# Optimization experiments

Measured on AMD Instinct MI355X. Metric: run time of the kernel, lower is better.

The kernel has to match this reference:

```python
import jax, jax.numpy as jnp
import numpy as np

EPS = 1e-3  # keras LayerNormalization default epsilon


def layer_norm(x, g, b):
    mu = jnp.mean(x, axis=-1, keepdims=True)
    var = jnp.mean(jnp.square(x - mu), axis=-1, keepdims=True)
    return g * (x - mu) / jnp.sqrt(var + EPS) + b


def setup_inputs() -> dict:
    key = jax.random.key(0)
    ks = jax.random.split(key, 16)
    B, S, E, H, F = 2, 4096, 512, 8, 2048
    s_e = 1.0 / np.sqrt(E)
    s_f = 1.0 / np.sqrt(F)
    inp = {
        "x": jax.random.normal(ks[0], (B, S, E), dtype=jnp.float32),
        "WQ": jax.random.normal(ks[1], (E, E), dtype=jnp.float32) * s_e,
        "bQ": jnp.zeros((E,), jnp.float32),
        "WK": jax.random.normal(ks[2], (E, E), dtype=jnp.float32) * s_e,
        "bK": jnp.zeros((E,), jnp.float32),
        "WV": jax.random.normal(ks[3], (E, E), dtype=jnp.float32) * s_e,
        "bV": jnp.zeros((E,), jnp.float32),
        "WO": jax.random.normal(ks[4], (E, E), dtype=jnp.float32) * s_e,
        "bO": jnp.zeros((E,), jnp.float32),
        "W1": jax.random.normal(ks[5], (E, F), dtype=jnp.float32) * s_e,
        "b1": jnp.zeros((F,), jnp.float32),
        "W2": jax.random.normal(ks[6], (F, E), dtype=jnp.float32) * s_f,
        "b2": jnp.zeros((E,), jnp.float32),
        "g1": jnp.ones((E,), jnp.float32),
        "beta1": jnp.zeros((E,), jnp.float32),
        "g2": jnp.ones((E,), jnp.float32),
        "beta2": jnp.zeros((E,), jnp.float32),
        "num_head": 8,
    }
    return inp


def reference(x, WQ, bQ, WK, bK, WV, bV, WO, bO, W1, b1, W2, b2,
              g1, beta1, g2, beta2, num_head):
    B, S, E = x.shape
    H = num_head
    d = E // H
    scale = jnp.sqrt(jnp.asarray(d, jnp.float32))

    q = (x @ WQ + bQ).reshape(B, S, H, d).transpose(0, 2, 1, 3)  # [B,H,S,d]
    k = (x @ WK + bK).reshape(B, S, H, d).transpose(0, 2, 1, 3)
    v = (x @ WV + bV).reshape(B, S, H, d).transpose(0, 2, 1, 3)

    score = jnp.einsum('bhqd,bhkd->bhqk', q, k) / scale  # O(S^2) materialized, as in source
    attn = jax.nn.softmax(score, axis=-1)
    zs = jnp.einsum('bhqk,bhkd->bhqd', attn, v)  # [B,H,S,d]

    # Faithful to source bug: reshape [B,H,S,d] -> [B,S,E] WITHOUT transposing back
    zs = zs.reshape(B, S, E)
    zs = zs @ WO + bO

    z = layer_norm(zs + x, g1, beta1)
    r = jax.nn.relu(z @ W1 + b1) @ W2 + b2
    r = layer_norm(r + z, g2, beta2)
    return r
```

## Files before the change

### kernel.cpp

```cpp
#include <hip/hip_runtime.h>
#include <hip/hip_bf16.h>

typedef unsigned short u16;
typedef __attribute__((ext_vector_type(8))) short bf16x8;
typedef __attribute__((ext_vector_type(4))) float f32x4;
typedef __attribute__((ext_vector_type(16))) float f32x16;

static constexpr int BB = 2;
static constexpr int SS = 4096;
static constexpr int EE = 512;
static constexpr int HH = 8;
static constexpr int DD = 64;
static constexpr int FF = 2048;
static constexpr int NR = BB * SS;
static constexpr int QS = 3 * EE;

#define QSCALE 0.18033688011112042f

__device__ __forceinline__ u16 f2bf(float f) {
  union { float f; unsigned u; } v; v.f = f;
  unsigned r = v.u + 0x7FFFu + ((v.u >> 16) & 1u);
  return (u16)(r >> 16);
}
__device__ __forceinline__ unsigned pack2(float a, float b) {
  return (unsigned)f2bf(a) | ((unsigned)f2bf(b) << 16);
}
__device__ __forceinline__ float bf2f_lo(unsigned u) {
  union { unsigned u; float f; } v; v.u = u << 16; return v.f;
}
__device__ __forceinline__ float bf2f_hi(unsigned u) {
  union { unsigned u; float f; } v; v.u = u & 0xffff0000u; return v.f;
}
__device__ __forceinline__ unsigned cvtpk(float lo, float hi) {
  unsigned r;
  asm("v_cvt_pk_bf16_f32 %0, %1, %2" : "=v"(r) : "v"(lo), "v"(hi));
  return r;
}
__device__ __forceinline__ void perm32swap(unsigned& a, unsigned& b) {
  asm("v_permlane32_swap_b32 %0, %1" : "+v"(a), "+v"(b));
}
__device__ __forceinline__ void gload_lds16(const u16* g, u16* l) {
  __builtin_amdgcn_global_load_lds(
      (const __attribute__((address_space(1))) unsigned*)g,
      (__attribute__((address_space(3))) unsigned*)l, 16, 0, 0);
}

struct TrJob { const float* W; u16* Wt; int K, N, k0, n0; };

__device__ __forceinline__ void transp_tile(const float* W, u16* Wt, int K,
                                            int N, int k0, int n0, int t) {
  __shared__ float T[64][65];
  const int tn = t & 63, tk = t >> 6;
#pragma unroll
  for (int i = 0; i < 16; ++i) {
    int kk = tk * 16 + i;
    T[kk][tn] = W[(size_t)(k0 + kk) * N + n0 + tn];
  }
  __syncthreads();
#pragma unroll
  for (int i = 0; i < 16; ++i) {
    int nn = tk * 16 + i;
    Wt[(size_t)(n0 + nn) * K + k0 + tn] = f2bf(T[tn][nn]);
  }
}

__global__ __launch_bounds__(256) void prep_all(
    const float* __restrict__ x, u16* __restrict__ xb,
    const float* __restrict__ WQ, const float* __restrict__ WK,
    const float* __restrict__ WV, const float* __restrict__ WO,
    const float* __restrict__ W1, const float* __restrict__ W2,
    u16* __restrict__ Wqkv_t, u16* __restrict__ WO_t, u16* __restrict__ W1_t,
    u16* __restrict__ W2_t, const float* __restrict__ bQ,
    const float* __restrict__ bK, const float* __restrict__ bV,
    float* __restrict__ bqkv) {
  const int bx = blockIdx.x;
  const int t = threadIdx.x;
  if (bx < 2048) {
    int i = (bx * 256 + t) * 8;
    float4 a = *(const float4*)(x + i);
    float4 b = *(const float4*)(x + i + 4);
    uint4 u;
    u.x = pack2(a.x, a.y); u.y = pack2(a.z, a.w);
    u.z = pack2(b.x, b.y); u.w = pack2(b.z, b.w);
    *(uint4*)(xb + i) = u;
    return;
  }
  int idx = bx - 2048;
  if (idx < 768) {
    TrJob j;
    if (idx < 256) {
      const float* srcs[4] = {WQ, WK, WV, WO};
      u16* dsts[4] = {Wqkv_t, Wqkv_t + 512 * 512, Wqkv_t + 1024 * 512, WO_t};
      int w = idx >> 6, l = idx & 63;
      j = {srcs[w], dsts[w], 512, 512, (l & 7) * 64, (l >> 3) * 64};
    } else if (idx < 512) {
      int l = idx - 256;
      j = {W1, W1_t, 512, 2048, (l & 7) * 64, (l >> 3) * 64};
    } else {
      int l = idx - 512;
      j = {W2, W2_t, 2048, 512, (l & 31) * 64, (l >> 5) * 64};
    }
    transp_tile(j.W, j.Wt, j.K, j.N, j.k0, j.n0, t);
    return;
  }
  for (int i = t; i < QS; i += 256)
    bqkv[i] = i < 512 ? bQ[i] : (i < 1024 ? bK[i - 512] : bV[i - 1024]);
}

__global__ __launch_bounds__(256) void transp_v(const u16* __restrict__ qkvb,
                                                u16* __restrict__ vt) {
  __shared__ u16 T[64][72];
  const int s0 = blockIdx.x * 64, c0 = blockIdx.y * 64, b = blockIdx.z;
  const int t = threadIdx.x;
#pragma unroll
  for (int i = 0; i < 2; ++i) {
    int idx = t + i * 256;
    int row = idx >> 3, c8 = idx & 7;
    *(uint4*)(&T[row][c8 * 8]) = *(const uint4*)(
        &qkvb[((size_t)b * SS + s0 + row) * QS + 1024 + c0 + c8 * 8]);
  }
  __syncthreads();
#pragma unroll
  for (int i = 0; i < 2; ++i) {
    int idx = t + i * 256;
    int c = idx >> 3, s8 = idx & 7;
    u16 tmp[8];
#pragma unroll
    for (int j = 0; j < 8; ++j) tmp[j] = T[s8 * 8 + j][c];
    *(uint4*)(&vt[((size_t)b * EE + c0 + c) * SS + s0 + s8 * 8]) =
        *(uint4*)tmp;
  }
}

template <int RELU, int OUT_BF16, int SCALEQ = 0>
__global__ __launch_bounds__(256) void gemm64(
    const u16* __restrict__ A, const u16* __restrict__ Bt,
    const float* __restrict__ bias, void* __restrict__ Cout,
    int M, int N, int K) {
  __shared__ __align__(16) u16 As[2][64 * 64];
  __shared__ __align__(16) u16 Bs[2][64 * 64];
  const int t = threadIdx.x;
  const int lane = t & 63, wid = t >> 6;
  const int lm = lane & 15, lg = lane >> 4;
  const int bm = blockIdx.x * 64, bn = blockIdx.y * 64;
  const int wr = (wid >> 1) * 32, wc = (wid & 1) * 32;
  const int sr = lane >> 3;
  const int scb = (lane & 7) ^ sr;

  f32x4 acc[2][2];
#pragma unroll
  for (int i = 0; i < 2; ++i)
#pragma unroll
    for (int j = 0; j < 2; ++j) acc[i][j] = (f32x4){0.f, 0.f, 0.f, 0.f};

  auto stage = [&](int kb, int buf) {
#pragma unroll
    for (int i = 0; i < 2; ++i) {
      int r8 = wid * 16 + i * 8;
      gload_lds16(A + (size_t)(bm + r8 + sr) * K + kb + scb * 8,
                  &As[buf][r8 * 64]);
      gload_lds16(Bt + (size_t)(bn + r8 + sr) * K + kb + scb * 8,
                  &Bs[buf][r8 * 64]);
    }
  };

  stage(0, 0);
  const int nsteps = K >> 6;
  for (int s = 0; s < nsteps; ++s) {
    const int cur = s & 1;
    if (s + 1 < nsteps) {
      stage((s + 1) << 6, cur ^ 1);
      asm volatile("s_waitcnt vmcnt(4)" ::: "memory");
    } else {
      asm volatile("s_waitcnt vmcnt(0)" ::: "memory");
    }
    __builtin_amdgcn_sched_barrier(0);
    __builtin_amdgcn_s_barrier();

#pragma unroll
    for (int c = 0; c < 2; ++c) {
      bf16x8 af[2], bfr[2];
#pragma unroll
      for (int i = 0; i < 2; ++i) {
        int ar = wr + i * 16 + lm;
        af[i] = *(const bf16x8*)(
            &As[cur][ar * 64 + (((c * 4 + lg) ^ (ar & 7)) << 3)]);
        int br = wc + i * 16 + lm;
        bfr[i] = *(const bf16x8*)(
            &Bs[cur][br * 64 + (((c * 4 + lg) ^ (br & 7)) << 3)]);
      }
#pragma unroll
      for (int i = 0; i < 2; ++i)
#pragma unroll
        for (int j = 0; j < 2; ++j)
          acc[i][j] = __builtin_amdgcn_mfma_f32_16x16x32_bf16(
              af[i], bfr[j], acc[i][j], 0, 0, 0);
    }

    asm volatile("s_waitcnt lgkmcnt(0)" ::: "memory");
    __builtin_amdgcn_s_barrier();
  }

  float bi[2];
#pragma unroll
  for (int j = 0; j < 2; ++j) bi[j] = bias[bn + wc + j * 16 + lm];

#pragma unroll
  for (int i = 0; i < 2; ++i) {
#pragma unroll
    for (int j = 0; j < 2; ++j) {
      int col = bn + wc + j * 16 + lm;
#pragma unroll
      for (int r = 0; r < 4; ++r) {
        int row = bm + wr + i * 16 + lg * 4 + r;
        float vv = acc[i][j][r] + bi[j];
        if (RELU) vv = fmaxf(vv, 0.f);
        if (SCALEQ && col < 512) vv *= QSCALE;
        if (OUT_BF16)
          ((u16*)Cout)[(size_t)row * N + col] = f2bf(vv);
        else
          ((float*)Cout)[(size_t)row * N + col] = vv;
      }
    }
  }
}

__global__ __launch_bounds__(128, 4) void attn_split(
    const u16* __restrict__ qkv, const u16* __restrict__ vt,
    u16* __restrict__ po, float* __restrict__ pl) {
  __shared__ __align__(16) u16 K_lds[2][32 * 64];
  __shared__ __align__(16) u16 V_lds[2][64 * 32];

  const int bh = blockIdx.x;
  const int qblock = blockIdx.y;
  const int half = blockIdx.z;
  po += (size_t)half * (9u << 19);
  pl += (size_t)half * (1u << 18);
  const int b = bh >> 3, h = bh & 7;
  const int t = threadIdx.x;
  const int lane = t & 63, wid = t >> 6;
  const int q32 = lane & 31, hi = lane >> 5;
  const int qs7 = q32 & 7;
  const int vswz = (q32 & 3) ^ ((q32 >> 2) & 3);
  const size_t bS = (size_t)b * SS;
  const int koff0 = half * 2048;
  const u16* kp = qkv + 512;
  const u16* vrow = vt + ((size_t)b * EE + h * DD) * SS;
  const int qbase = qblock * 64 + wid * 32;

  bf16x8 qf[4];
  {
    const u16* qrow = qkv + (bS + qbase + q32) * QS + h * DD + hi * 8;
#pragma unroll
    for (int c = 0; c < 4; ++c) qf[c] = *(const bf16x8*)(qrow + c * 16);
  }

  const int sr = lane >> 3;
  const int scb = (lane & 7) ^ sr;
  const int vr = lane >> 2;
  const int vcb = (lane & 3) ^ (vr & 3) ^ ((vr >> 2) & 3);

  f32x16 o0, o1, z16;
#pragma unroll
  for (int i = 0; i < 16; ++i) { o0[i] = 0.f; o1[i] = 0.f; z16[i] = 0.f; }
  float lsum = 0.f;

  auto stage = [&](int kt, int bufi) {
#pragma unroll
    for (int i = 0; i < 2; ++i) {
      int rb = wid * 16 + i * 8;
      gload_lds16(
          kp + (bS + koff0 + kt * 32 + rb + sr) * QS + h * DD + scb * 8,
          &K_lds[bufi][rb * 64]);
    }
#pragma unroll
    for (int i = 0; i < 2; ++i) {
      int rb = wid * 32 + i * 16;
      gload_lds16(vrow + (size_t)(rb + vr) * SS + koff0 + kt * 32 + vcb * 8,
                  &V_lds[bufi][rb * 32]);
    }
  };

  stage(0, 0);

  constexpr int NT = 2048 / 32;
  for (int kt = 0; kt < NT; ++kt) {
    const int cur = kt & 1;
    if (kt + 1 < NT) {
      stage(kt + 1, cur ^ 1);
      asm volatile("s_waitcnt vmcnt(4)" ::: "memory");
    } else {
      asm volatile("s_waitcnt vmcnt(0)" ::: "memory");
    }
    __builtin_amdgcn_sched_barrier(0);
    __builtin_amdgcn_s_barrier();

    f32x16 s;
    __builtin_amdgcn_s_setprio(1);
    {
      bf16x8 kf = *(const bf16x8*)(
          &K_lds[cur][q32 * 64 + ((hi ^ qs7) << 3)]);
      s = __builtin_amdgcn_mfma_f32_32x32x16_bf16(kf, qf[0], z16, 0, 0, 0);
    }
#pragma unroll
    for (int c = 1; c < 4; ++c) {
      bf16x8 kf = *(const bf16x8*)(
          &K_lds[cur][q32 * 64 + (((2 * c + hi) ^ qs7) << 3)]);
      s = __builtin_amdgcn_mfma_f32_32x32x16_bf16(kf, qf[c], s, 0, 0, 0);
    }
    __builtin_amdgcn_s_setprio(0);
    float p[16];
#pragma unroll
    for (int r = 0; r < 16; ++r) {
      p[r] = __builtin_amdgcn_exp2f(s[r]);
      lsum += p[r];
    }

    __builtin_amdgcn_s_setprio(1);
#pragma unroll
    for (int kc = 0; kc < 2; ++kc) {
      const int rA = kc * 8, rB = rA + 4;
      unsigned wA0 = cvtpk(p[rA + 0], p[rA + 1]);
      unsigned wA1 = cvtpk(p[rA + 2], p[rA + 3]);
      unsigned wB0 = cvtpk(p[rB + 0], p[rB + 1]);
      unsigned wB1 = cvtpk(p[rB + 2], p[rB + 3]);
      perm32swap(wA0, wB0);
      perm32swap(wA1, wB1);
      union { unsigned u[4]; bf16x8 v; } pf;
      pf.u[0] = wA0; pf.u[1] = wA1; pf.u[2] = wB0; pf.u[3] = wB1;
      bf16x8 vf0 = *(const bf16x8*)(
          &V_lds[cur][q32 * 32 + (((2 * kc + hi) ^ vswz) << 3)]);
      bf16x8 vf1 = *(const bf16x8*)(
          &V_lds[cur][(32 + q32) * 32 + (((2 * kc + hi) ^ vswz) << 3)]);
      o0 = __builtin_amdgcn_mfma_f32_32x32x16_bf16(pf.v, vf0, o0, 0, 0, 0);
      o1 = __builtin_amdgcn_mfma_f32_32x32x16_bf16(pf.v, vf1, o1, 0, 0, 0);
    }
    __builtin_amdgcn_s_setprio(0);

    asm volatile("s_waitcnt lgkmcnt(0)" ::: "memory");
    __builtin_amdgcn_s_barrier();
  }

  float fl = lsum + __shfl_xor(lsum, 32);
  const size_t rowbase = (size_t)bh * 4096 + qbase;
  if (lane < 32) pl[rowbase + q32] = fl;
#pragma unroll
  for (int reg = 0; reg < 16; ++reg) {
    int q = (reg & 3) + 8 * (reg >> 2) + 4 * hi;
    u16* dst = po + (rowbase + q) * 64;
    dst[q32] = f2bf(o0[reg]);
    dst[32 + q32] = f2bf(o1[reg]);
  }
}

__global__ __launch_bounds__(256) void attn_combine(
    const u16* __restrict__ po0, const u16* __restrict__ po1,
    const float* __restrict__ pl0, const float* __restrict__ pl1,
    u16* __restrict__ zs) {
  const int row = blockIdx.x * 32 + (threadIdx.x >> 3);
  const int dblk = (threadIdx.x & 7) * 8;
  const int bh = row >> 12, s = row & 4095;
  const int b = bh >> 3, h = bh & 7;
  const float inv = 1.f / (pl0[row] + pl1[row]);
  uint4 a = *(const uint4*)(po0 + (size_t)row * 64 + dblk);
  uint4 c = *(const uint4*)(po1 + (size_t)row * 64 + dblk);
  uint4 r;
  r.x = pack2((bf2f_lo(a.x) + bf2f_lo(c.x)) * inv,
              (bf2f_hi(a.x) + bf2f_hi(c.x)) * inv);
  r.y = pack2((bf2f_lo(a.y) + bf2f_lo(c.y)) * inv,
              (bf2f_hi(a.y) + bf2f_hi(c.y)) * inv);
  r.z = pack2((bf2f_lo(a.z) + bf2f_lo(c.z)) * inv,
              (bf2f_hi(a.z) + bf2f_hi(c.z)) * inv);
  r.w = pack2((bf2f_lo(a.w) + bf2f_lo(c.w)) * inv,
              (bf2f_hi(a.w) + bf2f_hi(c.w)) * inv);
  u16* dst = zs + ((size_t)b * SS + h * 512 + (s >> 3)) * EE + (s & 7) * 64;
  *(uint4*)(dst + dblk) = r;
}

template <int WF32>
__global__ __launch_bounds__(128) void add_ln_b(
    const u16* __restrict__ a, const u16* __restrict__ xres,
    const float* __restrict__ g, const float* __restrict__ beta,
    u16* __restrict__ outb, float* __restrict__ outf) {
  const int row = blockIdx.x;
  const int tid = threadIdx.x;
  uint2 av = *(const uint2*)(a + (size_t)row * EE + tid * 4);
  uint2 xv = *(const uint2*)(xres + (size_t)row * EE + tid * 4);
  float vx = bf2f_lo(av.x) + bf2f_lo(xv.x);
  float vy = bf2f_hi(av.x) + bf2f_hi(xv.x);
  float vz = bf2f_lo(av.y) + bf2f_lo(xv.y);
  float vw = bf2f_hi(av.y) + bf2f_hi(xv.y);
  float sum = vx + vy + vz + vw;
  float sq = vx * vx + vy * vy + vz * vz + vw * vw;
#pragma unroll
  for (int off = 1; off < 64; off <<= 1) {
    sum += __shfl_xor(sum, off);
    sq += __shfl_xor(sq, off);
  }
  __shared__ float s0[2], s1[2];
  int w = tid >> 6;
  if ((tid & 63) == 0) { s0[w] = sum; s1[w] = sq; }
  __syncthreads();
  sum = s0[0] + s0[1];
  sq = s1[0] + s1[1];
  float mu = sum * (1.0f / EE);
  float var = sq * (1.0f / EE) - mu * mu;
  float r = rsqrtf(var + 1e-3f);
  int c = tid * 4;
  float4 gv = *(const float4*)(g + c);
  float4 bv = *(const float4*)(beta + c);
  float o0 = gv.x * (vx - mu) * r + bv.x;
  float o1 = gv.y * (vy - mu) * r + bv.y;
  float o2 = gv.z * (vz - mu) * r + bv.z;
  float o3 = gv.w * (vw - mu) * r + bv.w;
  if (WF32) {
    float4 ov = {o0, o1, o2, o3};
    *(float4*)(outf + (size_t)row * EE + c) = ov;
  } else {
    uint2 u;
    u.x = pack2(o0, o1);
    u.y = pack2(o2, o3);
    *(uint2*)(outb + (size_t)row * EE + c) = u;
  }
}

extern "C" void kernel_launch(void* const* d_in, const int* in_sizes, int n_in,
                              void* d_out, int out_size, void* d_ws,
                              size_t ws_size, hipStream_t stream) {
  const float* x = (const float*)d_in[0];
  const float* WQ = (const float*)d_in[1];
  const float* bQ = (const float*)d_in[2];
  const float* WK = (const float*)d_in[3];
  const float* bK = (const float*)d_in[4];
  const float* WV = (const float*)d_in[5];
  const float* bV = (const float*)d_in[6];
  const float* WO = (const float*)d_in[7];
  const float* bO = (const float*)d_in[8];
  const float* W1 = (const float*)d_in[9];
  const float* b1 = (const float*)d_in[10];
  const float* W2 = (const float*)d_in[11];
  const float* b2 = (const float*)d_in[12];
  const float* g1 = (const float*)d_in[13];
  const float* be1 = (const float*)d_in[14];
  const float* g2 = (const float*)d_in[15];
  const float* be2 = (const float*)d_in[16];
  float* out = (float*)d_out;

  const size_t MB = 1u << 20;
  char* w = (char*)d_ws;
  u16* Wqkv_t = (u16*)(w + 0);
  u16* WO_t   = (u16*)(w + 2 * MB);
  u16* W1_t   = (u16*)(w + 3 * MB);
  u16* W2_t   = (u16*)(w + 5 * MB);
  float* bqkv = (float*)(w + 7 * MB);
  u16* qkvb = (u16*)(w + 8 * MB);
  u16* zsb  = (u16*)(w + 32 * MB);
  u16* po0  = (u16*)(w + 40 * MB);
  u16* po1  = (u16*)(w + 49 * MB);
  float* pl0 = (float*)(w + 58 * MB);
  float* pl1 = (float*)(w + 59 * MB);
  u16* zs2b = (u16*)(w + 40 * MB);
  u16* f2b  = (u16*)(w + 49 * MB);
  u16* zb   = (u16*)(w + 72 * MB);
  u16* xb   = (u16*)(w + 80 * MB);
  u16* vtb  = (u16*)(w + 88 * MB);
  u16* f1   = (u16*)(w + 8 * MB);

  dim3 blk(256);

  prep_all<<<dim3(2817), blk, 0, stream>>>(x, xb, WQ, WK, WV, WO, W1, W2,
                                           Wqkv_t, WO_t, W1_t, W2_t, bQ, bK,
                                           bV, bqkv);
  gemm64<0, 1, 1><<<dim3(128, 24), blk, 0, stream>>>(xb, Wqkv_t, bqkv, qkvb,
                                                     NR, QS, EE);
  transp_v<<<dim3(SS / 64, EE / 64, BB), blk, 0, stream>>>(qkvb, vtb);
  attn_split<<<dim3(BB * HH, SS / 64, 2), dim3(128), 0, stream>>>(qkvb, vtb,
                                                                  po0, pl0);
  attn_combine<<<dim3(2048), blk, 0, stream>>>(po0, po1, pl0, pl1, zsb);
  gemm64<0, 1><<<dim3(128, 8), blk, 0, stream>>>(zsb, WO_t, bO, zs2b,
                                                 NR, EE, EE);
  add_ln_b<0><<<dim3(NR), dim3(128), 0, stream>>>(zs2b, xb, g1, be1, zb,
                                                  nullptr);
  gemm64<1, 1><<<dim3(128, 32), blk, 0, stream>>>(zb, W1_t, b1, f1,
                                                  NR, FF, EE);
  gemm64<0, 1><<<dim3(128, 8), blk, 0, stream>>>(f1, W2_t, b2, f2b,
                                                 NR, EE, FF);
  add_ln_b<1><<<dim3(NR), dim3(128), 0, stream>>>(f2b, zb, g2, be2, nullptr,
                                                  out);
}
```

Before: 217.1 us.

## Add 128x128 GEMM tile for QKV and FFN1, compute softmax row sums via MFMA

Introduces a 128x128-tile GEMM kernel (single-buffered LDS, 4x4 MFMA 16x16x32 per wave) and uses it for the QKV projection and the first FFN GEMM, raising data reuse per loaded tile. In attention, the per-lane exp-sum accumulation plus shuffle is replaced by an extra MFMA against an all-ones B operand, so row sums come out of the matrix unit instead of VALU adds. The larger tile drops double buffering and uses more registers, and the extra MFMA adds matrix-unit work in the attention inner loop.

```diff
diff --git a/kernel.cpp b/kernel.cpp
--- a/kernel.cpp
+++ b/kernel.cpp
@@ -133,6 +133,82 @@
 }
 
 template <int RELU, int OUT_BF16, int SCALEQ = 0>
+__global__ __launch_bounds__(256) void gemm128(
+    const u16* __restrict__ A, const u16* __restrict__ Bt,
+    const float* __restrict__ bias, void* __restrict__ Cout,
+    int M, int N, int K) {
+  __shared__ __align__(16) u16 As[128 * 64];
+  __shared__ __align__(16) u16 Bs[128 * 64];
+  const int t = threadIdx.x;
+  const int lane = t & 63, wid = t >> 6;
+  const int lm = lane & 15, lg = lane >> 4;
+  const int bm = blockIdx.x * 128, bn = blockIdx.y * 128;
+  const int wr = (wid >> 1) * 64, wc = (wid & 1) * 64;
+  const int sr = lane >> 3;
+  const int scb = (lane & 7) ^ sr;
+
+  f32x4 acc[4][4];
+#pragma unroll
+  for (int i = 0; i < 4; ++i)
+#pragma unroll
+    for (int j = 0; j < 4; ++j) acc[i][j] = (f32x4){0.f, 0.f, 0.f, 0.f};
+
+  for (int kb = 0; kb < K; kb += 64) {
+    __syncthreads();
+#pragma unroll
+    for (int i = 0; i < 4; ++i) {
+      int rr = wid * 32 + i * 8 + sr;
+      gload_lds16(A + (size_t)(bm + rr) * K + kb + scb * 8,
+                  &As[(wid * 32 + i * 8) * 64]);
+      gload_lds16(Bt + (size_t)(bn + rr) * K + kb + scb * 8,
+                  &Bs[(wid * 32 + i * 8) * 64]);
+    }
+    __syncthreads();
+
+#pragma unroll
+    for (int c = 0; c < 2; ++c) {
+      bf16x8 af[4], bfr[4];
+#pragma unroll
+      for (int i = 0; i < 4; ++i) {
+        int ar = wr + i * 16 + lm;
+        af[i] = *(const bf16x8*)(&As[ar * 64 + (((c * 4 + lg) ^ (ar & 7)) << 3)]);
+        int br = wc + i * 16 + lm;
+        bfr[i] = *(const bf16x8*)(&Bs[br * 64 + (((c * 4 + lg) ^ (br & 7)) << 3)]);
+      }
+#pragma unroll
+      for (int i = 0; i < 4; ++i)
+#pragma unroll
+        for (int j = 0; j < 4; ++j)
+          acc[i][j] = __builtin_amdgcn_mfma_f32_16x16x32_bf16(
+              af[i], bfr[j], acc[i][j], 0, 0, 0);
+    }
+  }
+
+  float bi[4];
+#pragma unroll
+  for (int j = 0; j < 4; ++j) bi[j] = bias[bn + wc + j * 16 + lm];
+
+#pragma unroll
+  for (int i = 0; i < 4; ++i) {
+#pragma unroll
+    for (int j = 0; j < 4; ++j) {
+      int col = bn + wc + j * 16 + lm;
+#pragma unroll
+      for (int r = 0; r < 4; ++r) {
+        int row = bm + wr + i * 16 + lg * 4 + r;
+        float vv = acc[i][j][r] + bi[j];
+        if (RELU) vv = fmaxf(vv, 0.f);
+        if (SCALEQ && col < 512) vv *= QSCALE;
+        if (OUT_BF16)
+          ((u16*)Cout)[(size_t)row * N + col] = f2bf(vv);
+        else
+          ((float*)Cout)[(size_t)row * N + col] = vv;
+      }
+    }
+  }
+}
+
+template <int RELU, int OUT_BF16, int SCALEQ = 0>
 __global__ __launch_bounds__(256) void gemm64(
     const u16* __restrict__ A, const u16* __restrict__ Bt,
     const float* __restrict__ bias, void* __restrict__ Cout,
@@ -254,16 +330,20 @@
 #pragma unroll
     for (int c = 0; c < 4; ++c) qf[c] = *(const bf16x8*)(qrow + c * 16);
   }
+  bf16x8 onesf;
+#pragma unroll
+  for (int i = 0; i < 8; ++i) onesf[i] = (short)0x3F80;
 
   const int sr = lane >> 3;
   const int scb = (lane & 7) ^ sr;
   const int vr = lane >> 2;
   const int vcb = (lane & 3) ^ (vr & 3) ^ ((vr >> 2) & 3);
 
-  f32x16 o0, o1, z16;
-#pragma unroll
-  for (int i = 0; i < 16; ++i) { o0[i] = 0.f; o1[i] = 0.f; z16[i] = 0.f; }
-  float lsum = 0.f;
+  f32x16 o0, o1, ol, z16;
+#pragma unroll
+  for (int i = 0; i < 16; ++i) {
+    o0[i] = 0.f; o1[i] = 0.f; ol[i] = 0.f; z16[i] = 0.f;
+  }
 
   auto stage = [&](int kt, int bufi) {
 #pragma unroll
@@ -311,10 +391,7 @@
     __builtin_amdgcn_s_setprio(0);
     float p[16];
 #pragma unroll
-    for (int r = 0; r < 16; ++r) {
-      p[r] = __builtin_amdgcn_exp2f(s[r]);
-      lsum += p[r];
-    }
+    for (int r = 0; r < 16; ++r) p[r] = __builtin_amdgcn_exp2f(s[r]);
 
     __builtin_amdgcn_s_setprio(1);
 #pragma unroll
@@ -334,6 +411,7 @@
           &V_lds[cur][(32 + q32) * 32 + (((2 * kc + hi) ^ vswz) << 3)]);
       o0 = __builtin_amdgcn_mfma_f32_32x32x16_bf16(pf.v, vf0, o0, 0, 0, 0);
       o1 = __builtin_amdgcn_mfma_f32_32x32x16_bf16(pf.v, vf1, o1, 0, 0, 0);
+      ol = __builtin_amdgcn_mfma_f32_32x32x16_bf16(pf.v, onesf, ol, 0, 0, 0);
     }
     __builtin_amdgcn_s_setprio(0);
 
@@ -341,12 +419,11 @@
     __builtin_amdgcn_s_barrier();
   }
 
-  float fl = lsum + __shfl_xor(lsum, 32);
   const size_t rowbase = (size_t)bh * 4096 + qbase;
-  if (lane < 32) pl[rowbase + q32] = fl;
 #pragma unroll
   for (int reg = 0; reg < 16; ++reg) {
     int q = (reg & 3) + 8 * (reg >> 2) + 4 * hi;
+    if (q32 == q) pl[rowbase + q] = ol[reg];
     u16* dst = po + (rowbase + q) * 64;
     dst[q32] = f2bf(o0[reg]);
     dst[32 + q32] = f2bf(o1[reg]);
@@ -471,7 +548,7 @@
   prep_all<<<dim3(2817), blk, 0, stream>>>(x, xb, WQ, WK, WV, WO, W1, W2,
                                            Wqkv_t, WO_t, W1_t, W2_t, bQ, bK,
                                            bV, bqkv);
-  gemm64<0, 1, 1><<<dim3(128, 24), blk, 0, stream>>>(xb, Wqkv_t, bqkv, qkvb,
+  gemm128<0, 1, 1><<<dim3(64, 12), blk, 0, stream>>>(xb, Wqkv_t, bqkv, qkvb,
                                                      NR, QS, EE);
   transp_v<<<dim3(SS / 64, EE / 64, BB), blk, 0, stream>>>(qkvb, vtb);
   attn_split<<<dim3(BB * HH, SS / 64, 2), dim3(128), 0, stream>>>(qkvb, vtb,
@@ -481,7 +558,7 @@
                                                  NR, EE, EE);
   add_ln_b<0><<<dim3(NR), dim3(128), 0, stream>>>(zs2b, xb, g1, be1, zb,
                                                   nullptr);
-  gemm64<1, 1><<<dim3(128, 32), blk, 0, stream>>>(zb, W1_t, b1, f1,
+  gemm128<1, 1><<<dim3(64, 16), blk, 0, stream>>>(zb, W1_t, b1, f1,
                                                   NR, FF, EE);
   gemm64<0, 1><<<dim3(128, 8), blk, 0, stream>>>(f1, W2_t, b2, f2b,
                                                  NR, EE, FF);
```

Result: no change. 219.8 us (+1.2%).
